# Kernel optimization log

Measured on AMD Instinct MI355X. Metric: run time of the kernel, lower is better.

## Reference

```python
import jax, jax.numpy as jnp
import numpy as np

EPS = 1e-5

def layernorm(x, w, b):
    m = jnp.mean(x, axis=-1, keepdims=True)
    v = jnp.var(x, axis=-1, keepdims=True)
    return (x - m) * jax.lax.rsqrt(v + EPS) * w + b

def setup_inputs() -> dict:
    key = jax.random.key(0)
    ks = jax.random.split(key, 20)
    B, N, D, H, C = 4, 2048, 512, 8, 3
    HID = int(D * 4.0 * (2.0 / 3.0))  # SwiGLU hidden = 1365
    g = lambda k, shape, s: (jax.random.normal(k, shape, jnp.float32) * s)
    return {
        "x": g(ks[0], (B, N, D), 1.0),
        "coords": jax.random.uniform(ks[1], (B, N, C), jnp.float32),
        "ln1_w": jnp.ones((D,), jnp.float32),
        "ln1_b": jnp.zeros((D,), jnp.float32),
        "ln2_w": jnp.ones((D,), jnp.float32),
        "ln2_b": jnp.zeros((D,), jnp.float32),
        "Wqkv": g(ks[2], (D, 3 * D), D ** -0.5),
        "bqkv": jnp.zeros((3 * D,), jnp.float32),
        "Wo": g(ks[3], (D, D), D ** -0.5),
        "bo": jnp.zeros((D,), jnp.float32),
        "Wc": g(ks[4], (C, H), 0.1),
        "bc": jnp.zeros((H,), jnp.float32),
        "W1": g(ks[5], (D, HID), D ** -0.5),
        "b1": jnp.zeros((HID,), jnp.float32),
        "W2": g(ks[6], (D, HID), D ** -0.5),
        "b2": jnp.zeros((HID,), jnp.float32),
        "W3": g(ks[7], (HID, D), HID ** -0.5),
        "b3": jnp.zeros((D,), jnp.float32),
    }

def reference(x, coords, ln1_w, ln1_b, ln2_w, ln2_b, Wqkv, bqkv, Wo, bo,
              Wc, bc, W1, b1, W2, b2, W3, b3):
    B, N, D = x.shape
    H = bc.shape[0]
    dh = D // H
    # --- coord-aware patch attention (pre-norm) ---
    h = layernorm(x, ln1_w, ln1_b)
    qkv = h @ Wqkv + bqkv                                # [B,N,3D]
    q, k, v = jnp.split(qkv, 3, axis=-1)
    to_heads = lambda t: t.reshape(B, N, H, dh).transpose(0, 2, 1, 3)  # [B,H,N,dh]
    q, k, v = to_heads(q), to_heads(k), to_heads(v)
    scores = jnp.einsum("bhnd,bhmd->bhnm", q, k) / np.sqrt(dh)
    rel = coords[:, :, None, :] - coords[:, None, :, :]  # [B,N,N,C]
    bias = jnp.einsum("bnmc,ch->bhnm", rel, Wc) + bc[None, :, None, None]
    attn = jax.nn.softmax(scores + bias, axis=-1)
    o = jnp.einsum("bhnm,bhmd->bhnd", attn, v)
    o = o.transpose(0, 2, 1, 3).reshape(B, N, D)
    x = x + (o @ Wo + bo)                                # residual 1
    # --- SwiGLU FFN (pre-norm) ---
    h2 = layernorm(x, ln2_w, ln2_b)
    ff = jax.nn.silu(h2 @ W1 + b1) * (h2 @ W2 + b2)
    x = x + (ff @ W3 + b3)                               # residual 2
    return x
```

## Files before the change

kernel.cpp:

```cpp
#include <hip/hip_runtime.h>
#include <hip/hip_bf16.h>
#include <math.h>

#define B_   4
#define N_   2048
#define D_   512
#define H_   8
#define DH_  64
#define C_   3
#define HID_ 1365
#define HIDP 1408
#define ROWS_ (B_*N_)
#define TD_  (3*D_)

typedef __attribute__((ext_vector_type(8))) short short8;
typedef __attribute__((ext_vector_type(4))) float floatx4;

#define MFMA16(a,b,c) __builtin_amdgcn_mfma_f32_16x16x32_bf16(a,b,c,0,0,0)

typedef __attribute__((address_space(3))) unsigned lds_u32;
typedef __attribute__((address_space(1))) unsigned glb_u32;

__device__ __forceinline__ short sh(float v){
  union { __hip_bfloat16 b; short s; } u;
  u.b = __float2bfloat16(v);
  return u.s;
}

__device__ __forceinline__ int swz(int col, int row){
  return (col & ~63) | (col & 7) | ((((col >> 3) & 7) ^ (row & 7)) << 3);
}

template<int ROWS, int PITCH>
__device__ __forceinline__ void stageG(short* __restrict__ lds,
    const short* __restrict__ g, int ldg, int t){
  const int LPR = PITCH/8;
  const int RPI = 64/LPR;
  const int PW  = (ROWS/RPI)/4;
  int lane = t & 63, w = t >> 6;
  #pragma unroll
  for (int i = 0; i < PW; ++i){
    int r0  = (w*PW + i)*RPI;
    int row = r0 + lane/LPR;
    const short* ga = g + (size_t)row*ldg + (lane % LPR)*8;
    short* la = lds + r0*PITCH;
    __builtin_amdgcn_global_load_lds((const glb_u32*)ga, (lds_u32*)la, 16, 0, 0);
  }
}

__device__ __forceinline__ short8 fragS(const short* __restrict__ lds, int pitch,
    int mbase, int lane, int kk){
  int row  = mbase + (lane & 15);
  int seg  = (kk >> 3) + (lane >> 4);
  int phys = seg ^ (row & 7);
  return *(const short8*)(lds + row*pitch + phys*8);
}

__device__ __forceinline__ short8 fragP(const short* __restrict__ lds,
    int mbase, int lane, int kk){
  return *(const short8*)(lds + (mbase + (lane & 15))*136 + kk + ((lane >> 4) << 3));
}

__global__ __launch_bounds__(256) void convT_all(
    const float* __restrict__ Wqkv, const float* __restrict__ Wo,
    const float* __restrict__ W1, const float* __restrict__ W2,
    const float* __restrict__ W3,
    short* __restrict__ Wtqkv, short* __restrict__ Wto,
    short* __restrict__ Wt1, short* __restrict__ Wt2, short* __restrict__ Wt3,
    const float* __restrict__ coords, const float* __restrict__ Wc,
    float* __restrict__ tv){
  __shared__ float tile[32][33];
  int id = blockIdx.x;
  int t = threadIdx.x;
  if (id >= 3136){
    int idx = (id - 3136)*256 + t;
    int n = idx & (N_-1);
    int hh = (idx >> 11) & (H_-1);
    int b = idx >> 14;
    float s = 0.f;
    #pragma unroll
    for (int cc = 0; cc < C_; ++cc)
      s += coords[((size_t)(b*N_+n))*C_ + cc] * Wc[cc*H_ + hh];
    tv[idx] = s;
    return;
  }
  const float* in; short* out; int K, NN, Kp, nx;
  if (id < 768)      { in=Wqkv; out=Wtqkv; K=512;  NN=1536; Kp=512;  nx=48; }
  else if (id < 1024){ in=Wo;   out=Wto;   K=512;  NN=512;  Kp=512;  nx=16; id-=768; }
  else if (id < 1728){ in=W1;   out=Wt1;   K=512;  NN=HID_; Kp=512;  nx=44; id-=1024; }
  else if (id < 2432){ in=W2;   out=Wt2;   K=512;  NN=HID_; Kp=512;  nx=44; id-=1728; }
  else               { in=W3;   out=Wt3;   K=HID_; NN=512;  Kp=HIDP; nx=16; id-=2432; }
  int nt0 = (id % nx)*32, kt0 = (id / nx)*32;
  int r = t >> 5, cc = t & 31;
  #pragma unroll
  for (int i=0;i<4;++i){
    int k = kt0 + i*8 + r, n = nt0 + cc;
    tile[i*8+r][cc] = (k<K && n<NN) ? in[(size_t)k*NN + n] : 0.f;
  }
  __syncthreads();
  #pragma unroll
  for (int i=0;i<4;++i){
    int n = nt0 + i*8 + r, k = kt0 + cc;
    out[(size_t)n*Kp + swz(k, n)] = sh(tile[cc][i*8+r]);
  }
}

__global__ __launch_bounds__(256) void ln_kernel(const float* __restrict__ x,
        const float* __restrict__ w, const float* __restrict__ b,
        short* __restrict__ out){
  int row = blockIdx.x;
  size_t base = (size_t)row * D_;
  int t = threadIdx.x;
  float v0 = x[base + t];
  float v1 = x[base + t + 256];
  float s  = v0 + v1;
  float s2 = v0*v0 + v1*v1;
  #pragma unroll
  for (int off = 32; off >= 1; off >>= 1){
    s  += __shfl_xor(s,  off, 64);
    s2 += __shfl_xor(s2, off, 64);
  }
  __shared__ float red[8];
  int lane = t & 63, wv = t >> 6;
  if (lane == 0){ red[wv] = s; red[4+wv] = s2; }
  __syncthreads();
  float sum  = red[0]+red[1]+red[2]+red[3];
  float sum2 = red[4]+red[5]+red[6]+red[7];
  float mean = sum * (1.0f/D_);
  float var  = sum2 * (1.0f/D_) - mean*mean;
  float inv  = rsqrtf(fmaxf(var, 0.f) + 1e-5f);
  out[base + swz(t,     row)] = sh((v0-mean)*inv*w[t]     + b[t]);
  out[base + swz(t+256, row)] = sh((v1-mean)*inv*w[t+256] + b[t+256]);
}

__global__ __launch_bounds__(256) void qkv_gemm(
    const short* __restrict__ A, const short* __restrict__ Bt,
    const float* __restrict__ bias,
    short* __restrict__ qb, short* __restrict__ kb, short* __restrict__ vbt){
  __shared__ short As[128*64];
  __shared__ short Bs[128*64];
  int t = threadIdx.x;
  int lane = t & 63, w = t >> 6;
  int wr = (w >> 1) * 64, wc = (w & 1) * 64;
  int col0 = blockIdx.x * 128, row0 = blockIdx.y * 128;
  floatx4 acc[4][4];
  #pragma unroll
  for (int mt=0;mt<4;++mt)
    #pragma unroll
    for (int nt=0;nt<4;++nt) acc[mt][nt] = (floatx4){0.f,0.f,0.f,0.f};
  for (int k0 = 0; k0 < D_; k0 += 64){
    __syncthreads();
    stageG<128,64>(As, A  + (size_t)row0*D_ + k0, D_, t);
    stageG<128,64>(Bs, Bt + (size_t)col0*D_ + k0, D_, t);
    __syncthreads();
    #pragma unroll
    for (int kk = 0; kk < 64; kk += 32){
      short8 af[4], bf[4];
      #pragma unroll
      for (int mt=0;mt<4;++mt) af[mt] = fragS(As, 64, wr+mt*16, lane, kk);
      #pragma unroll
      for (int nt=0;nt<4;++nt) bf[nt] = fragS(Bs, 64, wc+nt*16, lane, kk);
      #pragma unroll
      for (int mt=0;mt<4;++mt)
        #pragma unroll
        for (int nt=0;nt<4;++nt)
          acc[mt][nt] = MFMA16(af[mt], bf[nt], acc[mt][nt]);
    }
  }
  int quad = lane >> 4, c = lane & 15;
  #pragma unroll
  for (int mt=0;mt<4;++mt){
    #pragma unroll
    for (int nt=0;nt<4;++nt){
      #pragma unroll
      for (int r=0;r<4;++r){
        int row = row0 + wr + mt*16 + quad*4 + r;
        int col = col0 + wc + nt*16 + c;
        float v = acc[mt][nt][r] + bias[col];
        int bidx = row >> 11, n = row & (N_-1);
        int which = col >> 9, d = col & (D_-1), hh = d >> 6, hd = d & 63;
        short sv = sh(v);
        if (which == 0)
          qb[(((size_t)(bidx*H_ + hh))*N_ + n)*DH_ + swz(hd, n)] = sv;
        else if (which == 1)
          kb[(((size_t)(bidx*H_ + hh))*N_ + n)*DH_ + swz(hd, n)] = sv;
        else
          vbt[(((size_t)(bidx*H_ + hh))*DH_ + hd)*N_ + swz(n, hd)] = sv;
      }
    }
  }
}

__global__ __launch_bounds__(256) void gemm64(
    const short* __restrict__ A, int lda,
    const short* __restrict__ Bt, int Ktot,
    const float* __restrict__ bias,
    const float* __restrict__ resid, float* __restrict__ outF){
  __shared__ short As[128*64];
  __shared__ short Bs[64*64];
  int t = threadIdx.x, lane = t & 63, w = t >> 6;
  int wr = w * 32;
  int col0 = blockIdx.x * 64, row0 = blockIdx.y * 128;
  floatx4 acc[2][4];
  #pragma unroll
  for (int mt=0;mt<2;++mt)
    #pragma unroll
    for (int nt=0;nt<4;++nt) acc[mt][nt] = (floatx4){0.f,0.f,0.f,0.f};
  for (int k0 = 0; k0 < Ktot; k0 += 64){
    __syncthreads();
    stageG<128,64>(As, A  + (size_t)row0*lda + k0, lda, t);
    stageG<64,64> (Bs, Bt + (size_t)col0*Ktot + k0, Ktot, t);
    __syncthreads();
    #pragma unroll
    for (int kk = 0; kk < 64; kk += 32){
      short8 af[2], bf[4];
      #pragma unroll
      for (int mt=0;mt<2;++mt) af[mt] = fragS(As, 64, wr+mt*16, lane, kk);
      #pragma unroll
      for (int nt=0;nt<4;++nt) bf[nt] = fragS(Bs, 64, nt*16, lane, kk);
      #pragma unroll
      for (int mt=0;mt<2;++mt)
        #pragma unroll
        for (int nt=0;nt<4;++nt)
          acc[mt][nt] = MFMA16(af[mt], bf[nt], acc[mt][nt]);
    }
  }
  int quad = lane >> 4, c = lane & 15;
  #pragma unroll
  for (int mt=0;mt<2;++mt){
    #pragma unroll
    for (int nt=0;nt<4;++nt){
      #pragma unroll
      for (int r=0;r<4;++r){
        int row = row0 + wr + mt*16 + quad*4 + r;
        int col = col0 + nt*16 + c;
        size_t idx = (size_t)row*D_ + col;
        outF[idx] = acc[mt][nt][r] + bias[col] + resid[idx];
      }
    }
  }
}

__global__ __launch_bounds__(256) void gate_gemm(
    const short* __restrict__ A,
    const short* __restrict__ Bt1, const short* __restrict__ Bt2,
    const float* __restrict__ b1, const float* __restrict__ b2,
    short* __restrict__ ff){
  __shared__ short As[128*64];
  __shared__ short B1s[64*64];
  __shared__ short B2s[64*64];
  int t = threadIdx.x, lane = t & 63, w = t >> 6;
  int wr = (w >> 1) * 64, wc = (w & 1) * 32;
  int col0 = blockIdx.x * 64, row0 = blockIdx.y * 128;
  floatx4 a1[4][2], a2[4][2];
  #pragma unroll
  for (int mt=0;mt<4;++mt)
    #pragma unroll
    for (int nt=0;nt<2;++nt){
      a1[mt][nt] = (floatx4){0.f,0.f,0.f,0.f};
      a2[mt][nt] = (floatx4){0.f,0.f,0.f,0.f};
    }
  for (int k0 = 0; k0 < D_; k0 += 64){
    __syncthreads();
    stageG<128,64>(As, A + (size_t)row0*D_ + k0, D_, t);
    stageG<64,64>(B1s, Bt1 + (size_t)col0*D_ + k0, D_, t);
    stageG<64,64>(B2s, Bt2 + (size_t)col0*D_ + k0, D_, t);
    __syncthreads();
    #pragma unroll
    for (int kk = 0; kk < 64; kk += 32){
      short8 af[4], f1[2], f2[2];
      #pragma unroll
      for (int mt=0;mt<4;++mt) af[mt] = fragS(As, 64, wr+mt*16, lane, kk);
      #pragma unroll
      for (int nt=0;nt<2;++nt){
        f1[nt] = fragS(B1s, 64, wc+nt*16, lane, kk);
        f2[nt] = fragS(B2s, 64, wc+nt*16, lane, kk);
      }
      #pragma unroll
      for (int mt=0;mt<4;++mt)
        #pragma unroll
        for (int nt=0;nt<2;++nt){
          a1[mt][nt] = MFMA16(af[mt], f1[nt], a1[mt][nt]);
          a2[mt][nt] = MFMA16(af[mt], f2[nt], a2[mt][nt]);
        }
    }
  }
  int quad = lane >> 4, c = lane & 15;
  #pragma unroll
  for (int mt=0;mt<4;++mt){
    #pragma unroll
    for (int nt=0;nt<2;++nt){
      #pragma unroll
      for (int r=0;r<4;++r){
        int row = row0 + wr + mt*16 + quad*4 + r;
        int col = col0 + wc + nt*16 + c;
        float g1 = a1[mt][nt][r] + (col < HID_ ? b1[col] : 0.f);
        float g2 = a2[mt][nt][r] + (col < HID_ ? b2[col] : 0.f);
        float sig = 1.f / (1.f + __expf(-g1));
        ff[(size_t)row*HIDP + swz(col, row)] = sh(g1*sig*g2);
      }
    }
  }
}

__global__ __launch_bounds__(256) void attn_mfma(
    const short* __restrict__ qb, const short* __restrict__ kb,
    const short* __restrict__ vbt, const float* __restrict__ tv,
    short* __restrict__ o){
  __shared__ short Ks[128*64];
  __shared__ short Vt[64*128];
  __shared__ short Ps[128*136];
  __shared__ float tsh[128];
  int qt = blockIdx.x, h = blockIdx.y, b = blockIdx.z;
  int bh = b*H_ + h;
  int t = threadIdx.x, lane = t & 63, w = t >> 6;
  int quad = lane >> 4, c = lane & 15;
  stageG<128,64>(Ps, qb + ((size_t)bh*N_ + qt*128)*DH_, DH_, t);
  __syncthreads();
  short8 qf[2][2];
  #pragma unroll
  for (int mt=0;mt<2;++mt)
    #pragma unroll
    for (int kh=0;kh<2;++kh)
      qf[mt][kh] = fragS(Ps, 64, w*32 + mt*16, lane, kh*32);

  floatx4 O[2][4];
  float l_i[2][4];
  #pragma unroll
  for (int mt=0;mt<2;++mt){
    #pragma unroll
    for (int nt=0;nt<4;++nt) O[mt][nt] = (floatx4){0.f,0.f,0.f,0.f};
    #pragma unroll
    for (int r=0;r<4;++r) l_i[mt][r] = 0.f;
  }
  const short* Kbase = kb  + (size_t)bh*N_*DH_;
  const short* Vbase = vbt + (size_t)bh*DH_*N_;

  for (int kt = 0; kt < N_/128; ++kt){
    __syncthreads();
    stageG<128,64>(Ks, Kbase + (size_t)kt*128*DH_, DH_, t);
    stageG<64,128>(Vt, Vbase + kt*128, N_, t);
    if (t < 128) tsh[t] = tv[(size_t)bh*N_ + kt*128 + t];
    __syncthreads();

    floatx4 S[2][8];
    #pragma unroll
    for (int mt=0;mt<2;++mt)
      #pragma unroll
      for (int nt=0;nt<8;++nt) S[mt][nt] = (floatx4){0.f,0.f,0.f,0.f};
    #pragma unroll
    for (int kh=0;kh<2;++kh){
      short8 kf[8];
      #pragma unroll
      for (int nt=0;nt<8;++nt) kf[nt] = fragS(Ks, 64, nt*16, lane, kh*32);
      #pragma unroll
      for (int mt=0;mt<2;++mt)
        #pragma unroll
        for (int nt=0;nt<8;++nt)
          S[mt][nt] = MFMA16(qf[mt][kh], kf[nt], S[mt][nt]);
    }
    float ts[8];
    #pragma unroll
    for (int nt=0;nt<8;++nt) ts[nt] = tsh[nt*16 + c];
    #pragma unroll
    for (int mt=0;mt<2;++mt)
      #pragma unroll
      for (int r=0;r<4;++r){
        #pragma unroll
        for (int nt=0;nt<8;++nt){
          float p = __expf(S[mt][nt][r]*0.125f - ts[nt]);
          l_i[mt][r] += p;
          Ps[(w*32 + mt*16 + quad*4 + r)*136 + nt*16 + c] = sh(p);
        }
      }
    asm volatile("s_waitcnt lgkmcnt(0)" ::: "memory");
    #pragma unroll
    for (int kh=0;kh<4;++kh){
      short8 vf[4], pf[2];
      #pragma unroll
      for (int nt=0;nt<4;++nt) vf[nt] = fragS(Vt, 128, nt*16, lane, kh*32);
      #pragma unroll
      for (int mt=0;mt<2;++mt) pf[mt] = fragP(Ps, w*32 + mt*16, lane, kh*32);
      #pragma unroll
      for (int mt=0;mt<2;++mt)
        #pragma unroll
        for (int nt=0;nt<4;++nt)
          O[mt][nt] = MFMA16(pf[mt], vf[nt], O[mt][nt]);
    }
  }
  #pragma unroll
  for (int mt=0;mt<2;++mt){
    #pragma unroll
    for (int r=0;r<4;++r){
      float l = l_i[mt][r];
      #pragma unroll
      for (int off=1; off<16; off<<=1) l += __shfl_xor(l, off, 64);
      float invl = 1.f / l;
      int row = qt*128 + w*32 + mt*16 + quad*4 + r;
      #pragma unroll
      for (int nt=0;nt<4;++nt){
        int col = h*DH_ + nt*16 + c;
        o[((size_t)(b*N_ + row))*D_ + swz(col, row)] = sh(O[mt][nt][r]*invl);
      }
    }
  }
}

extern "C" void kernel_launch(void* const* d_in, const int* in_sizes, int n_in,
                              void* d_out, int out_size, void* d_ws, size_t ws_size,
                              hipStream_t stream){
  const float* x      = (const float*)d_in[0];
  const float* coords = (const float*)d_in[1];
  const float* ln1_w  = (const float*)d_in[2];
  const float* ln1_b  = (const float*)d_in[3];
  const float* ln2_w  = (const float*)d_in[4];
  const float* ln2_b  = (const float*)d_in[5];
  const float* Wqkv   = (const float*)d_in[6];
  const float* bqkv   = (const float*)d_in[7];
  const float* Wo     = (const float*)d_in[8];
  const float* bo     = (const float*)d_in[9];
  const float* Wc     = (const float*)d_in[10];
  const float* W1     = (const float*)d_in[12];
  const float* b1     = (const float*)d_in[13];
  const float* W2     = (const float*)d_in[14];
  const float* b2     = (const float*)d_in[15];
  const float* W3     = (const float*)d_in[16];
  const float* b3     = (const float*)d_in[17];

  char* ws = (char*)d_ws;
  short* Wtqkv = (short*)(ws);
  short* Wto   = (short*)(ws + 1572864);
  short* Wt1   = (short*)(ws + 2097152);
  short* Wt2   = (short*)(ws + 3538944);
  short* Wt3   = (short*)(ws + 4980736);
  float* tv    = (float*)(ws + 6422528);
  short* h     = (short*)(ws + 6684672);
  short* qb    = (short*)(ws + 15073280);
  short* kb    = (short*)(ws + 23461888);
  short* vbt   = (short*)(ws + 31850496);
  short* o     = h;
  short* h2    = h;
  short* ff    = qb;
  float* x1    = (float*)d_out;

  convT_all<<<dim3(3392), dim3(256), 0, stream>>>(Wqkv, Wo, W1, W2, W3,
      Wtqkv, Wto, Wt1, Wt2, Wt3, coords, Wc, tv);
  ln_kernel<<<dim3(ROWS_), dim3(256), 0, stream>>>(x, ln1_w, ln1_b, h);
  qkv_gemm<<<dim3(12,64), dim3(256), 0, stream>>>(h, Wtqkv, bqkv, qb, kb, vbt);
  attn_mfma<<<dim3(16,8,4), dim3(256), 0, stream>>>(qb, kb, vbt, tv, o);
  gemm64<<<dim3(8,64), dim3(256), 0, stream>>>(o, 512, Wto, 512, bo, x, x1);
  ln_kernel<<<dim3(ROWS_), dim3(256), 0, stream>>>(x1, ln2_w, ln2_b, h2);
  gate_gemm<<<dim3(22,64), dim3(256), 0, stream>>>(h2, Wt1, Wt2, b1, b2, ff);
  gemm64<<<dim3(8,64), dim3(256), 0, stream>>>(ff, HIDP, Wt3, HIDP, b3, x1, x1);
}
```

Baseline: 317.5 us.

## Fold coordinate bias into V and compute softmax denominators with MFMA

Within each query row the coordinate bias reduces to a per-key term, so the per-key factor exp(-t_m) is folded into V when the QKV GEMM writes it. That factor is also stored as an extra V row, so the softmax row sum comes out of the PV MFMA instead of scalar accumulation and a shuffle reduction. The attention inner loop loses the per-key bias subtraction, the tsh staging and the l_i accumulation, at the cost of 25% more PV MFMAs, a larger padded V buffer with uninitialized pad rows, and bf16 rounding of the scale factor. Separately, gemm64 now uses 128-wide K tiles to halve its barrier and staging iterations, at the cost of more LDS.

```diff
diff --git a/kernel.cpp b/kernel.cpp
--- a/kernel.cpp
+++ b/kernel.cpp
@@ -12,6 +12,7 @@
 #define HIDP 1408
 #define ROWS_ (B_*N_)
 #define TD_  (3*D_)
+#define VROWS 80
 
 typedef __attribute__((ext_vector_type(8))) short short8;
 typedef __attribute__((ext_vector_type(4))) float floatx4;
@@ -68,7 +69,7 @@
     short* __restrict__ Wtqkv, short* __restrict__ Wto,
     short* __restrict__ Wt1, short* __restrict__ Wt2, short* __restrict__ Wt3,
     const float* __restrict__ coords, const float* __restrict__ Wc,
-    float* __restrict__ tv){
+    float* __restrict__ tv, short* __restrict__ vbt){
   __shared__ float tile[32][33];
   int id = blockIdx.x;
   int t = threadIdx.x;
@@ -82,6 +83,7 @@
     for (int cc = 0; cc < C_; ++cc)
       s += coords[((size_t)(b*N_+n))*C_ + cc] * Wc[cc*H_ + hh];
     tv[idx] = s;
+    vbt[((size_t)(b*H_+hh)*VROWS + 64)*N_ + n] = sh(__expf(-s));
     return;
   }
   const float* in; short* out; int K, NN, Kp, nx;
@@ -135,7 +137,7 @@
 
 __global__ __launch_bounds__(256) void qkv_gemm(
     const short* __restrict__ A, const short* __restrict__ Bt,
-    const float* __restrict__ bias,
+    const float* __restrict__ bias, const float* __restrict__ tv,
     short* __restrict__ qb, short* __restrict__ kb, short* __restrict__ vbt){
   __shared__ short As[128*64];
   __shared__ short Bs[128*64];
@@ -179,13 +181,14 @@
         float v = acc[mt][nt][r] + bias[col];
         int bidx = row >> 11, n = row & (N_-1);
         int which = col >> 9, d = col & (D_-1), hh = d >> 6, hd = d & 63;
-        short sv = sh(v);
         if (which == 0)
-          qb[(((size_t)(bidx*H_ + hh))*N_ + n)*DH_ + swz(hd, n)] = sv;
+          qb[(((size_t)(bidx*H_ + hh))*N_ + n)*DH_ + swz(hd, n)] = sh(v);
         else if (which == 1)
-          kb[(((size_t)(bidx*H_ + hh))*N_ + n)*DH_ + swz(hd, n)] = sv;
-        else
-          vbt[(((size_t)(bidx*H_ + hh))*DH_ + hd)*N_ + swz(n, hd)] = sv;
+          kb[(((size_t)(bidx*H_ + hh))*N_ + n)*DH_ + swz(hd, n)] = sh(v);
+        else {
+          float wv = __expf(-tv[((size_t)bidx*H_ + hh)*N_ + n]);
+          vbt[(((size_t)(bidx*H_ + hh))*VROWS + hd)*N_ + swz(n, hd)] = sh(v * wv);
+        }
       }
     }
   }
@@ -196,8 +199,8 @@
     const short* __restrict__ Bt, int Ktot,
     const float* __restrict__ bias,
     const float* __restrict__ resid, float* __restrict__ outF){
-  __shared__ short As[128*64];
-  __shared__ short Bs[64*64];
+  __shared__ short As[128*128];
+  __shared__ short Bs[64*128];
   int t = threadIdx.x, lane = t & 63, w = t >> 6;
   int wr = w * 32;
   int col0 = blockIdx.x * 64, row0 = blockIdx.y * 128;
@@ -206,18 +209,18 @@
   for (int mt=0;mt<2;++mt)
     #pragma unroll
     for (int nt=0;nt<4;++nt) acc[mt][nt] = (floatx4){0.f,0.f,0.f,0.f};
-  for (int k0 = 0; k0 < Ktot; k0 += 64){
-    __syncthreads();
-    stageG<128,64>(As, A  + (size_t)row0*lda + k0, lda, t);
-    stageG<64,64> (Bs, Bt + (size_t)col0*Ktot + k0, Ktot, t);
-    __syncthreads();
-    #pragma unroll
-    for (int kk = 0; kk < 64; kk += 32){
+  for (int k0 = 0; k0 < Ktot; k0 += 128){
+    __syncthreads();
+    stageG<128,128>(As, A  + (size_t)row0*lda + k0, lda, t);
+    stageG<64,128> (Bs, Bt + (size_t)col0*Ktot + k0, Ktot, t);
+    __syncthreads();
+    #pragma unroll
+    for (int kk = 0; kk < 128; kk += 32){
       short8 af[2], bf[4];
       #pragma unroll
-      for (int mt=0;mt<2;++mt) af[mt] = fragS(As, 64, wr+mt*16, lane, kk);
-      #pragma unroll
-      for (int nt=0;nt<4;++nt) bf[nt] = fragS(Bs, 64, nt*16, lane, kk);
+      for (int mt=0;mt<2;++mt) af[mt] = fragS(As, 128, wr+mt*16, lane, kk);
+      #pragma unroll
+      for (int nt=0;nt<4;++nt) bf[nt] = fragS(Bs, 128, nt*16, lane, kk);
       #pragma unroll
       for (int mt=0;mt<2;++mt)
         #pragma unroll
@@ -305,12 +308,10 @@
 
 __global__ __launch_bounds__(256) void attn_mfma(
     const short* __restrict__ qb, const short* __restrict__ kb,
-    const short* __restrict__ vbt, const float* __restrict__ tv,
-    short* __restrict__ o){
+    const short* __restrict__ vbt, short* __restrict__ o){
   __shared__ short Ks[128*64];
-  __shared__ short Vt[64*128];
+  __shared__ short Vt[VROWS*128];
   __shared__ short Ps[128*136];
-  __shared__ float tsh[128];
   int qt = blockIdx.x, h = blockIdx.y, b = blockIdx.z;
   int bh = b*H_ + h;
   int t = threadIdx.x, lane = t & 63, w = t >> 6;
@@ -324,23 +325,19 @@
     for (int kh=0;kh<2;++kh)
       qf[mt][kh] = fragS(Ps, 64, w*32 + mt*16, lane, kh*32);
 
-  floatx4 O[2][4];
-  float l_i[2][4];
-  #pragma unroll
-  for (int mt=0;mt<2;++mt){
-    #pragma unroll
-    for (int nt=0;nt<4;++nt) O[mt][nt] = (floatx4){0.f,0.f,0.f,0.f};
-    #pragma unroll
-    for (int r=0;r<4;++r) l_i[mt][r] = 0.f;
-  }
+  floatx4 O[2][5];
+  #pragma unroll
+  for (int mt=0;mt<2;++mt)
+    #pragma unroll
+    for (int nt=0;nt<5;++nt) O[mt][nt] = (floatx4){0.f,0.f,0.f,0.f};
+
   const short* Kbase = kb  + (size_t)bh*N_*DH_;
-  const short* Vbase = vbt + (size_t)bh*DH_*N_;
+  const short* Vbase = vbt + (size_t)bh*VROWS*N_;
 
   for (int kt = 0; kt < N_/128; ++kt){
     __syncthreads();
     stageG<128,64>(Ks, Kbase + (size_t)kt*128*DH_, DH_, t);
-    stageG<64,128>(Vt, Vbase + kt*128, N_, t);
-    if (t < 128) tsh[t] = tv[(size_t)bh*N_ + kt*128 + t];
+    stageG<VROWS,128>(Vt, Vbase + kt*128, N_, t);
     __syncthreads();
 
     floatx4 S[2][8];
@@ -359,32 +356,28 @@
         for (int nt=0;nt<8;++nt)
           S[mt][nt] = MFMA16(qf[mt][kh], kf[nt], S[mt][nt]);
     }
-    float ts[8];
-    #pragma unroll
-    for (int nt=0;nt<8;++nt) ts[nt] = tsh[nt*16 + c];
     #pragma unroll
     for (int mt=0;mt<2;++mt)
       #pragma unroll
       for (int r=0;r<4;++r){
         #pragma unroll
         for (int nt=0;nt<8;++nt){
-          float p = __expf(S[mt][nt][r]*0.125f - ts[nt]);
-          l_i[mt][r] += p;
+          float p = exp2f(S[mt][nt][r] * 0.18033688f);
           Ps[(w*32 + mt*16 + quad*4 + r)*136 + nt*16 + c] = sh(p);
         }
       }
     asm volatile("s_waitcnt lgkmcnt(0)" ::: "memory");
     #pragma unroll
     for (int kh=0;kh<4;++kh){
-      short8 vf[4], pf[2];
-      #pragma unroll
-      for (int nt=0;nt<4;++nt) vf[nt] = fragS(Vt, 128, nt*16, lane, kh*32);
+      short8 vf[5], pf[2];
+      #pragma unroll
+      for (int nt=0;nt<5;++nt) vf[nt] = fragS(Vt, 128, nt*16, lane, kh*32);
       #pragma unroll
       for (int mt=0;mt<2;++mt) pf[mt] = fragP(Ps, w*32 + mt*16, lane, kh*32);
       #pragma unroll
       for (int mt=0;mt<2;++mt)
         #pragma unroll
-        for (int nt=0;nt<4;++nt)
+        for (int nt=0;nt<5;++nt)
           O[mt][nt] = MFMA16(pf[mt], vf[nt], O[mt][nt]);
     }
   }
@@ -392,9 +385,7 @@
   for (int mt=0;mt<2;++mt){
     #pragma unroll
     for (int r=0;r<4;++r){
-      float l = l_i[mt][r];
-      #pragma unroll
-      for (int off=1; off<16; off<<=1) l += __shfl_xor(l, off, 64);
+      float l = __shfl(O[mt][4][r], (lane & 48), 64);
       float invl = 1.f / l;
       int row = qt*128 + w*32 + mt*16 + quad*4 + r;
       #pragma unroll
@@ -444,10 +435,10 @@
   float* x1    = (float*)d_out;
 
   convT_all<<<dim3(3392), dim3(256), 0, stream>>>(Wqkv, Wo, W1, W2, W3,
-      Wtqkv, Wto, Wt1, Wt2, Wt3, coords, Wc, tv);
+      Wtqkv, Wto, Wt1, Wt2, Wt3, coords, Wc, tv, vbt);
   ln_kernel<<<dim3(ROWS_), dim3(256), 0, stream>>>(x, ln1_w, ln1_b, h);
-  qkv_gemm<<<dim3(12,64), dim3(256), 0, stream>>>(h, Wtqkv, bqkv, qb, kb, vbt);
-  attn_mfma<<<dim3(16,8,4), dim3(256), 0, stream>>>(qb, kb, vbt, tv, o);
+  qkv_gemm<<<dim3(12,64), dim3(256), 0, stream>>>(h, Wtqkv, bqkv, tv, qb, kb, vbt);
+  attn_mfma<<<dim3(16,8,4), dim3(256), 0, stream>>>(qb, kb, vbt, o);
   gemm64<<<dim3(8,64), dim3(256), 0, stream>>>(o, 512, Wto, 512, bo, x, x1);
   ln_kernel<<<dim3(ROWS_), dim3(256), 0, stream>>>(x1, ln2_w, ln2_b, h2);
   gate_gemm<<<dim3(22,64), dim3(256), 0, stream>>>(h2, Wt1, Wt2, b1, b2, ff);
```

After: 337.9 us. +6.4%, slower.

## Halve attention query tile, fold LayerNorm1 into prep kernel, use exp2

Applied to the files above, without the earlier changes.

The attention kernel now handles 64 query rows per block instead of 128, doubling the grid to 1024 blocks and shrinking the P buffer in LDS. The aim is better occupancy and lower register pressure, at the cost of reloading each K/V tile twice as often. The first LayerNorm is merged into the weight-conversion launch as extra blocks, removing one kernel launch. The coordinate bias is prescaled by log2(e) so softmax can use exp2f with one fused multiply-add.

```diff
diff --git a/kernel.cpp b/kernel.cpp
--- a/kernel.cpp
+++ b/kernel.cpp
@@ -68,10 +68,36 @@
     short* __restrict__ Wtqkv, short* __restrict__ Wto,
     short* __restrict__ Wt1, short* __restrict__ Wt2, short* __restrict__ Wt3,
     const float* __restrict__ coords, const float* __restrict__ Wc,
-    float* __restrict__ tv){
-  __shared__ float tile[32][33];
+    float* __restrict__ tu,
+    const float* __restrict__ x, const float* __restrict__ ln1_w,
+    const float* __restrict__ ln1_b, short* __restrict__ h){
   int id = blockIdx.x;
   int t = threadIdx.x;
+  if (id >= 3392){
+    int row = id - 3392;
+    size_t base = (size_t)row * D_;
+    float v0 = x[base + t];
+    float v1 = x[base + t + 256];
+    float s  = v0 + v1;
+    float s2 = v0*v0 + v1*v1;
+    #pragma unroll
+    for (int off = 32; off >= 1; off >>= 1){
+      s  += __shfl_xor(s,  off, 64);
+      s2 += __shfl_xor(s2, off, 64);
+    }
+    __shared__ float red[8];
+    int lane = t & 63, wv = t >> 6;
+    if (lane == 0){ red[wv] = s; red[4+wv] = s2; }
+    __syncthreads();
+    float sum  = red[0]+red[1]+red[2]+red[3];
+    float sum2 = red[4]+red[5]+red[6]+red[7];
+    float mean = sum * (1.0f/D_);
+    float var  = sum2 * (1.0f/D_) - mean*mean;
+    float inv  = rsqrtf(fmaxf(var, 0.f) + 1e-5f);
+    h[base + swz(t,     row)] = sh((v0-mean)*inv*ln1_w[t]     + ln1_b[t]);
+    h[base + swz(t+256, row)] = sh((v1-mean)*inv*ln1_w[t+256] + ln1_b[t+256]);
+    return;
+  }
   if (id >= 3136){
     int idx = (id - 3136)*256 + t;
     int n = idx & (N_-1);
@@ -81,9 +107,10 @@
     #pragma unroll
     for (int cc = 0; cc < C_; ++cc)
       s += coords[((size_t)(b*N_+n))*C_ + cc] * Wc[cc*H_ + hh];
-    tv[idx] = s;
+    tu[idx] = s * 1.44269504f;
     return;
   }
+  __shared__ float tile[32][33];
   const float* in; short* out; int K, NN, Kp, nx;
   if (id < 768)      { in=Wqkv; out=Wtqkv; K=512;  NN=1536; Kp=512;  nx=48; }
   else if (id < 1024){ in=Wo;   out=Wto;   K=512;  NN=512;  Kp=512;  nx=16; id-=768; }
@@ -305,34 +332,30 @@
 
 __global__ __launch_bounds__(256) void attn_mfma(
     const short* __restrict__ qb, const short* __restrict__ kb,
-    const short* __restrict__ vbt, const float* __restrict__ tv,
+    const short* __restrict__ vbt, const float* __restrict__ tu,
     short* __restrict__ o){
   __shared__ short Ks[128*64];
   __shared__ short Vt[64*128];
-  __shared__ short Ps[128*136];
-  __shared__ float tsh[128];
+  __shared__ short Ps[64*136];
+  __shared__ float ush[128];
   int qt = blockIdx.x, h = blockIdx.y, b = blockIdx.z;
   int bh = b*H_ + h;
   int t = threadIdx.x, lane = t & 63, w = t >> 6;
   int quad = lane >> 4, c = lane & 15;
-  stageG<128,64>(Ps, qb + ((size_t)bh*N_ + qt*128)*DH_, DH_, t);
+  stageG<64,64>(Ps, qb + ((size_t)bh*N_ + qt*64)*DH_, DH_, t);
   __syncthreads();
-  short8 qf[2][2];
-  #pragma unroll
-  for (int mt=0;mt<2;++mt)
-    #pragma unroll
-    for (int kh=0;kh<2;++kh)
-      qf[mt][kh] = fragS(Ps, 64, w*32 + mt*16, lane, kh*32);
-
-  floatx4 O[2][4];
-  float l_i[2][4];
-  #pragma unroll
-  for (int mt=0;mt<2;++mt){
-    #pragma unroll
-    for (int nt=0;nt<4;++nt) O[mt][nt] = (floatx4){0.f,0.f,0.f,0.f};
-    #pragma unroll
-    for (int r=0;r<4;++r) l_i[mt][r] = 0.f;
-  }
+  short8 qf[2];
+  #pragma unroll
+  for (int kh=0;kh<2;++kh)
+    qf[kh] = fragS(Ps, 64, w*16, lane, kh*32);
+
+  floatx4 O[4];
+  float l_i[4];
+  #pragma unroll
+  for (int nt=0;nt<4;++nt) O[nt] = (floatx4){0.f,0.f,0.f,0.f};
+  #pragma unroll
+  for (int r=0;r<4;++r) l_i[r] = 0.f;
+
   const short* Kbase = kb  + (size_t)bh*N_*DH_;
   const short* Vbase = vbt + (size_t)bh*DH_*N_;
 
@@ -340,68 +363,50 @@
     __syncthreads();
     stageG<128,64>(Ks, Kbase + (size_t)kt*128*DH_, DH_, t);
     stageG<64,128>(Vt, Vbase + kt*128, N_, t);
-    if (t < 128) tsh[t] = tv[(size_t)bh*N_ + kt*128 + t];
-    __syncthreads();
-
-    floatx4 S[2][8];
-    #pragma unroll
-    for (int mt=0;mt<2;++mt)
-      #pragma unroll
-      for (int nt=0;nt<8;++nt) S[mt][nt] = (floatx4){0.f,0.f,0.f,0.f};
+    if (t < 128) ush[t] = tu[(size_t)bh*N_ + kt*128 + t];
+    __syncthreads();
+
+    floatx4 S[8];
+    #pragma unroll
+    for (int nt=0;nt<8;++nt) S[nt] = (floatx4){0.f,0.f,0.f,0.f};
     #pragma unroll
     for (int kh=0;kh<2;++kh){
-      short8 kf[8];
-      #pragma unroll
-      for (int nt=0;nt<8;++nt) kf[nt] = fragS(Ks, 64, nt*16, lane, kh*32);
-      #pragma unroll
-      for (int mt=0;mt<2;++mt)
-        #pragma unroll
-        for (int nt=0;nt<8;++nt)
-          S[mt][nt] = MFMA16(qf[mt][kh], kf[nt], S[mt][nt]);
-    }
-    float ts[8];
-    #pragma unroll
-    for (int nt=0;nt<8;++nt) ts[nt] = tsh[nt*16 + c];
-    #pragma unroll
-    for (int mt=0;mt<2;++mt)
-      #pragma unroll
-      for (int r=0;r<4;++r){
-        #pragma unroll
-        for (int nt=0;nt<8;++nt){
-          float p = __expf(S[mt][nt][r]*0.125f - ts[nt]);
-          l_i[mt][r] += p;
-          Ps[(w*32 + mt*16 + quad*4 + r)*136 + nt*16 + c] = sh(p);
-        }
+      #pragma unroll
+      for (int nt=0;nt<8;++nt)
+        S[nt] = MFMA16(qf[kh], fragS(Ks, 64, nt*16, lane, kh*32), S[nt]);
+    }
+    float u8[8];
+    #pragma unroll
+    for (int nt=0;nt<8;++nt) u8[nt] = ush[nt*16 + c];
+    #pragma unroll
+    for (int r=0;r<4;++r){
+      #pragma unroll
+      for (int nt=0;nt<8;++nt){
+        float p = exp2f(fmaf(S[nt][r], 0.18033688f, -u8[nt]));
+        l_i[r] += p;
+        Ps[(w*16 + quad*4 + r)*136 + nt*16 + c] = sh(p);
       }
+    }
     asm volatile("s_waitcnt lgkmcnt(0)" ::: "memory");
     #pragma unroll
     for (int kh=0;kh<4;++kh){
-      short8 vf[4], pf[2];
-      #pragma unroll
-      for (int nt=0;nt<4;++nt) vf[nt] = fragS(Vt, 128, nt*16, lane, kh*32);
-      #pragma unroll
-      for (int mt=0;mt<2;++mt) pf[mt] = fragP(Ps, w*32 + mt*16, lane, kh*32);
-      #pragma unroll
-      for (int mt=0;mt<2;++mt)
-        #pragma unroll
-        for (int nt=0;nt<4;++nt)
-          O[mt][nt] = MFMA16(pf[mt], vf[nt], O[mt][nt]);
-    }
-  }
-  #pragma unroll
-  for (int mt=0;mt<2;++mt){
-    #pragma unroll
-    for (int r=0;r<4;++r){
-      float l = l_i[mt][r];
-      #pragma unroll
-      for (int off=1; off<16; off<<=1) l += __shfl_xor(l, off, 64);
-      float invl = 1.f / l;
-      int row = qt*128 + w*32 + mt*16 + quad*4 + r;
-      #pragma unroll
-      for (int nt=0;nt<4;++nt){
-        int col = h*DH_ + nt*16 + c;
-        o[((size_t)(b*N_ + row))*D_ + swz(col, row)] = sh(O[mt][nt][r]*invl);
-      }
+      short8 pf = fragP(Ps, w*16, lane, kh*32);
+      #pragma unroll
+      for (int nt=0;nt<4;++nt)
+        O[nt] = MFMA16(pf, fragS(Vt, 128, nt*16, lane, kh*32), O[nt]);
+    }
+  }
+  #pragma unroll
+  for (int r=0;r<4;++r){
+    float l = l_i[r];
+    #pragma unroll
+    for (int off=1; off<16; off<<=1) l += __shfl_xor(l, off, 64);
+    float invl = 1.f / l;
+    int row = qt*64 + w*16 + quad*4 + r;
+    #pragma unroll
+    for (int nt=0;nt<4;++nt){
+      int col = h*DH_ + nt*16 + c;
+      o[((size_t)(b*N_ + row))*D_ + swz(col, row)] = sh(O[nt][r]*invl);
     }
   }
 }
@@ -433,7 +438,7 @@
   short* Wt1   = (short*)(ws + 2097152);
   short* Wt2   = (short*)(ws + 3538944);
   short* Wt3   = (short*)(ws + 4980736);
-  float* tv    = (float*)(ws + 6422528);
+  float* tu    = (float*)(ws + 6422528);
   short* h     = (short*)(ws + 6684672);
   short* qb    = (short*)(ws + 15073280);
   short* kb    = (short*)(ws + 23461888);
@@ -443,11 +448,10 @@
   short* ff    = qb;
   float* x1    = (float*)d_out;
 
-  convT_all<<<dim3(3392), dim3(256), 0, stream>>>(Wqkv, Wo, W1, W2, W3,
-      Wtqkv, Wto, Wt1, Wt2, Wt3, coords, Wc, tv);
-  ln_kernel<<<dim3(ROWS_), dim3(256), 0, stream>>>(x, ln1_w, ln1_b, h);
+  convT_all<<<dim3(11584), dim3(256), 0, stream>>>(Wqkv, Wo, W1, W2, W3,
+      Wtqkv, Wto, Wt1, Wt2, Wt3, coords, Wc, tu, x, ln1_w, ln1_b, h);
   qkv_gemm<<<dim3(12,64), dim3(256), 0, stream>>>(h, Wtqkv, bqkv, qb, kb, vbt);
-  attn_mfma<<<dim3(16,8,4), dim3(256), 0, stream>>>(qb, kb, vbt, tv, o);
+  attn_mfma<<<dim3(32,8,4), dim3(256), 0, stream>>>(qb, kb, vbt, tu, o);
   gemm64<<<dim3(8,64), dim3(256), 0, stream>>>(o, 512, Wto, 512, bo, x, x1);
   ln_kernel<<<dim3(ROWS_), dim3(256), 0, stream>>>(x1, ln2_w, ln2_b, h2);
   gate_gemm<<<dim3(22,64), dim3(256), 0, stream>>>(h2, Wt1, Wt2, b1, b2, ff);
```

Result: slower. 332.8 us (+4.8%).
